# Optimization experiments

Measured on AMD Instinct MI355X. Metric: run time of the kernel, lower is better.

Reference implementation:

```python
import jax, jax.numpy as jnp
import numpy as np

# --- module hyperparams (match init_kwargs) ---
IN_F, OUT_F, K, GROUP, STRIDE, PAD = 64, 64, 3, 8, 1, 1
NUM_KERNELS = int(np.ceil(OUT_F / GROUP))          # 8 groups
IN_DPC = int(np.ceil(IN_F / NUM_KERNELS))          # in-ch per group = 8
WORKING = GROUP * NUM_KERNELS                      # 64 conv out channels
WORKING_IN = IN_DPC * NUM_KERNELS                  # 64 conv in channels
B, H, W = 16, 192, 192


def setup_inputs() -> dict:
    key = jax.random.key(0)
    k1, k2, k3, k4, k5, k6 = jax.random.split(key, 6)
    x = jax.random.normal(k1, (B, IN_F, H, W), jnp.float32)
    # grouped conv weight, torch layout (out, in/groups, kh, kw), no bias
    conv_w = jax.random.normal(k2, (WORKING, WORKING_IN // NUM_KERNELS, K, K), jnp.float32) * 0.05
    A = jax.random.uniform(k3, (1, WORKING, 1, 1), jnp.float32)
    D = jax.random.uniform(k4, (1, WORKING, 1, 1), jnp.float32)
    bias = jax.random.uniform(k5, (1, WORKING, 1, 1), jnp.float32)
    perm = jax.random.permutation(k6, WORKING).astype(jnp.int32)  # torch.randperm buffer
    return {"x": x, "conv_w": conv_w, "A": A, "D": D, "bias": bias, "perm": perm}


def reference(x, conv_w, A, D, bias, perm):
    # channel pad to working_in (no-op for these dims, kept for fidelity)
    z = jnp.pad(x, ((0, 0), (0, WORKING_IN - IN_F), (0, 0), (0, 0)))
    # grouped conv2d, no bias
    z = jax.lax.conv_general_dilated(
        z, conv_w,
        window_strides=(STRIDE, STRIDE),
        padding=((PAD, PAD), (PAD, PAD)),
        dimension_numbers=("NCHW", "OIHW", "NCHW"),
        feature_group_count=NUM_KERNELS,
    )
    z = z * A                      # elementwise scale
    z = jnp.fft.fft(z, axis=1)     # FFT along channel dim -> complex64
    z = z * D                      # diagonal (real) scale in frequency space
    z = jnp.fft.ifft(z, axis=1)    # back to 'channel' space (still complex)
    z = z + bias
    # channel permutation gather, slice to out_f, normalize
    z = jnp.take(z, perm, axis=1)[:, :OUT_F]
    return z / jnp.sqrt(jnp.float32(OUT_F))
```

## Files before the change

kernel.cpp:

```cpp
#include <hip/hip_runtime.h>
#include <math.h>

#define Bn 16
#define Cn 64
#define Hn 192
#define Wn 192
#define NPIX (Bn * Cn * Hn * Wn)
#define NBLKS 256
#define ROWS 12
#define SLOTB (194 * 128)

typedef short bf16x8 __attribute__((ext_vector_type(8)));
typedef float f32x4 __attribute__((ext_vector_type(4)));
typedef __attribute__((address_space(1))) const unsigned int as1_u32;
typedef __attribute__((address_space(3))) unsigned int as3_u32;

__device__ __align__(16) unsigned short g_Ms[9 * 64 * 64];
__device__ __align__(16) float g_b2[64];

static __device__ __forceinline__ unsigned short f2bf(float f) {
    union { float f; unsigned u; } x; x.f = f;
    unsigned r = x.u + 0x7fffu + ((x.u >> 16) & 1u);
    return (unsigned short)(r >> 16);
}

__global__ void acdc_precompute(const float* __restrict__ cw, const float* __restrict__ A,
                                const float* __restrict__ D, const float* __restrict__ bias,
                                const int* __restrict__ perm) {
    __shared__ float mre[64];
    int p = blockIdx.x;
    int t = threadIdx.x;
    if (t < 64) {
        float re = 0.f;
        for (int k = 0; k < 64; ++k) {
            int a = (k * t) & 63;
            re += D[k] * cosf((float)a * 0.0981747704246810387f);
        }
        mre[t] = re;
    }
    __syncthreads();
    int pp = perm[p];
    for (int k0 = t; k0 < 576; k0 += 256) {
        int sp = k0 >> 6, c = k0 & 63;
        int g = c >> 3, cil = c & 7;
        float val = 0.f;
        for (int o = 0; o < 8; ++o) {
            int oc = g * 8 + o;
            float gco = mre[(pp - oc + 64) & 63] * A[oc] * (0.125f / 64.0f);
            val += gco * cw[(oc * 8 + cil) * 9 + sp];
        }
        g_Ms[((sp * 64 + p) << 6) + (((g ^ (p & 7)) << 3) | cil)] = f2bf(val);
    }
    if (p == 0 && t < 64)
        g_b2[t] = bias[perm[t]] * 0.125f;
}

__global__ __launch_bounds__(1024)
void acdc_main(const float* __restrict__ x, float* __restrict__ out) {
    __shared__ __align__(16) unsigned short Mlds[9 * 64 * 64];
    __shared__ __align__(16) unsigned char xsb[3 * SLOTB];

    int tid = threadIdx.x;
    int lane = tid & 63, wv = tid >> 6;
    int Lb = (blockIdx.x & 7) * (NBLKS / 8) + (blockIdx.x >> 3);
    int bb = Lb >> 4;
    int h0 = (Lb & 15) * ROWS;

    #pragma unroll
    for (int k = 0; k < 5; ++k) {
        int chunk = wv + k * 16;
        if (chunk < 72) {
            const unsigned char* src = (const unsigned char*)g_Ms + chunk * 1024 + lane * 16;
            __builtin_amdgcn_global_load_lds((as1_u32*)(const void*)src,
                (as3_u32*)(void*)((unsigned char*)Mlds + chunk * 1024), 16, 0, 0);
        }
    }

    int pxw = lane & 15, q = lane >> 4, rlane = lane & 15;
    int m = wv >> 2;
    int ng = wv & 3;

    const float* xb = x + (size_t)bb * Cn * Hn * Wn;

    float4 va[2], vb[2];
    auto xload = [&](int gh) {
        bool ok = (unsigned)gh < (unsigned)Hn;
        int ghc = ok ? gh : 0;
        #pragma unroll
        for (int k = 0; k < 2; ++k) {
            int idx = tid + (k << 10);
            va[k] = (float4){0.f, 0.f, 0.f, 0.f};
            vb[k] = (float4){0.f, 0.f, 0.f, 0.f};
            if (idx < 1600) {
                int f = idx % 50;
                int cp = idx / 50;
                if (ok && f >= 1 && f <= 48) {
                    const float* r0 = xb + ((size_t)(2 * cp) * Hn + ghc) * Wn + (f * 4 - 4);
                    va[k] = *(const float4*)r0;
                    vb[k] = *(const float4*)(r0 + Hn * Wn);
                }
            }
        }
    };
    auto xwrite = [&](int slot) {
        #pragma unroll
        for (int k = 0; k < 2; ++k) {
            int idx = tid + (k << 10);
            if (idx >= 1600) break;
            int f = idx % 50;
            int cp = idx / 50;
            int chunk = cp >> 2, sub = (cp & 3) * 4;
            float v0[4] = {va[k].x, va[k].y, va[k].z, va[k].w};
            float v1[4] = {vb[k].x, vb[k].y, vb[k].z, vb[k].w};
            #pragma unroll
            for (int j = 0; j < 4; ++j) {
                int c2 = f * 4 - 3 + j;
                if ((unsigned)c2 >= 194u) continue;
                unsigned u;
                asm("v_cvt_pk_bf16_f32 %0, %1, %2" : "=v"(u) : "v"(v0[j]), "v"(v1[j]));
                int key = (c2 + (c2 >> 3) + 3 * slot) & 7;
                int byte = slot * SLOTB + c2 * 128 + ((chunk ^ key) << 4) + sub;
                *(unsigned*)(xsb + byte) = u;
            }
        }
    };

    xload(h0 - 1); xwrite(0);
    xload(h0);     xwrite(1);
    xload(h0 + 1); xwrite(2);
    __syncthreads();

    int sA = 0;
    for (int t = 0; t < ROWS; ++t) {
        int h = h0 + t;
        int sB = sA + 1; if (sB == 3) sB = 0;
        int sC = sB + 1; if (sC == 3) sC = 0;
        if (t < ROWS - 1) xload(h + 2);

        f32x4 acc[3];
        #pragma unroll
        for (int i = 0; i < 3; ++i) acc[i] = (f32x4){0.f, 0.f, 0.f, 0.f};

        #pragma unroll
        for (int sp = 0; sp < 9; ++sp) {
            const int dy = sp / 3, dx = sp % 3;
            int slotr = (dy == 0) ? sA : (dy == 1) ? sB : sC;
            int sb = slotr * SLOTB;
            int s3 = 3 * slotr;
            int c2b = ng * 16 + pxw + dx;
            #pragma unroll
            for (int kh = 0; kh < 2; ++kh) {
                int ksl = kh * 4 + q;
                bf16x8 am = *(const bf16x8*)((const unsigned char*)Mlds + sp * 8192 +
                             rlane * 128 + ((ksl ^ (rlane & 7)) << 4) + m * 2048);
                bf16x8 bfr[3];
                #pragma unroll
                for (int i = 0; i < 3; ++i) {
                    int c2 = c2b + i * 64;
                    int key = (c2 + (c2 >> 3) + s3) & 7;
                    bfr[i] = *(const bf16x8*)(xsb + sb + c2 * 128 + ((ksl ^ key) << 4));
                }
                __builtin_amdgcn_s_setprio(1);
                #pragma unroll
                for (int i = 0; i < 3; ++i)
                    acc[i] = __builtin_amdgcn_mfma_f32_16x16x32_bf16(am, bfr[i], acc[i], 0, 0, 0);
                __builtin_amdgcn_s_setprio(0);
            }
        }

        {
            int rbase = m * 16 + q * 4;
            float4 bq = *(const float4*)(g_b2 + rbase);
            float bvs[4] = {bq.x, bq.y, bq.z, bq.w};
            #pragma unroll
            for (int i = 0; i < 3; ++i) {
                int px = (ng + i * 4) * 16 + pxw;
                #pragma unroll
                for (int j = 0; j < 4; ++j)
                    out[(((size_t)(bb * Cn + rbase + j)) * Hn + h) * Wn + px] =
                        acc[i][j] + bvs[j];
            }
        }

        __syncthreads();
        if (t < ROWS - 1) xwrite(sA);
        __syncthreads();
        sA = sB;
    }
}

extern "C" void kernel_launch(void* const* d_in, const int* in_sizes, int n_in,
                              void* d_out, int out_size, void* d_ws, size_t ws_size,
                              hipStream_t stream) {
    const float* x    = (const float*)d_in[0];
    const float* cw   = (const float*)d_in[1];
    const float* A    = (const float*)d_in[2];
    const float* D    = (const float*)d_in[3];
    const float* bias = (const float*)d_in[4];
    const int*   perm = (const int*)d_in[5];

    acdc_precompute<<<dim3(64), dim3(256), 0, stream>>>(cw, A, D, bias, perm);
    acdc_main<<<dim3(NBLKS), dim3(1024), 0, stream>>>(x, (float*)d_out);
}
```

Baseline: 92.16 us.

## Split row bands into column halves and compute four rows per step

The grid doubles to 512 blocks, and each block now covers a 96-column half of a 12-row band. Each iteration computes four output rows at once: waves are assigned per row, and each wave handles two M tiles against three pixel tiles. The ring grows to six LDS slots and is refilled four rows at a time, so there are 3 iterations instead of 12. This cuts barrier and loop overhead and reuses each A fragment across more MFMAs. The cost is extra halo columns at the split, scalar edge loads and more registers.

Measured after the change: 166.9 us. 1.81x slower.

```diff
diff --git a/kernel.cpp b/kernel.cpp
--- a/kernel.cpp
+++ b/kernel.cpp
@@ -6,9 +6,9 @@
 #define Hn 192
 #define Wn 192
 #define NPIX (Bn * Cn * Hn * Wn)
-#define NBLKS 256
-#define ROWS 12
-#define SLOTB (194 * 128)
+#define NBLKS 512
+#define WCOLS 98
+#define SLOTB (WCOLS * 128)
 
 typedef short bf16x8 __attribute__((ext_vector_type(8)));
 typedef float f32x4 __attribute__((ext_vector_type(4)));
@@ -58,13 +58,16 @@
 __global__ __launch_bounds__(1024)
 void acdc_main(const float* __restrict__ x, float* __restrict__ out) {
     __shared__ __align__(16) unsigned short Mlds[9 * 64 * 64];
-    __shared__ __align__(16) unsigned char xsb[3 * SLOTB];
+    __shared__ __align__(16) unsigned char xsb[6 * SLOTB];
 
     int tid = threadIdx.x;
     int lane = tid & 63, wv = tid >> 6;
     int Lb = (blockIdx.x & 7) * (NBLKS / 8) + (blockIdx.x >> 3);
-    int bb = Lb >> 4;
-    int h0 = (Lb & 15) * ROWS;
+    int bb = Lb >> 5;
+    int band = (Lb >> 1) & 15;
+    int half = Lb & 1;
+    int h0 = band * 12;
+    int cbase = half * 96;
 
     #pragma unroll
     for (int k = 0; k < 5; ++k) {
@@ -77,115 +80,173 @@
     }
 
     int pxw = lane & 15, q = lane >> 4, rlane = lane & 15;
-    int m = wv >> 2;
-    int ng = wv & 3;
+    int r = wv & 3;
+    int mg = (wv >> 2) & 1;
+    int ngg = wv >> 3;
 
     const float* xb = x + (size_t)bb * Cn * Hn * Wn;
 
-    float4 va[2], vb[2];
-    auto xload = [&](int gh) {
-        bool ok = (unsigned)gh < (unsigned)Hn;
-        int ghc = ok ? gh : 0;
+    for (int k = 0; k < 5; ++k) {
+        int idx = tid + (k << 10);
+        if (idx >= 4992) break;
+        int f = idx % 26;
+        int rr = (idx / 26) % 6;
+        int cp = idx / 156;
+        int gi = h0 - 1 + rr;
+        int gc0 = cbase - 4 + 4 * f;
+        float av[4] = {0.f, 0.f, 0.f, 0.f}, bv[4] = {0.f, 0.f, 0.f, 0.f};
+        bool giok = (unsigned)gi < (unsigned)Hn;
+        const float* r0 = xb + ((size_t)(2 * cp) * Hn + (giok ? gi : 0)) * Wn;
+        const float* r1 = r0 + Hn * Wn;
+        if (giok) {
+            if (gc0 >= 0 && gc0 <= Wn - 4) {
+                float4 a = *(const float4*)(r0 + gc0);
+                float4 b = *(const float4*)(r1 + gc0);
+                av[0]=a.x; av[1]=a.y; av[2]=a.z; av[3]=a.w;
+                bv[0]=b.x; bv[1]=b.y; bv[2]=b.z; bv[3]=b.w;
+            } else {
+                #pragma unroll
+                for (int j = 0; j < 4; ++j) {
+                    int gc = gc0 + j;
+                    if ((unsigned)gc < (unsigned)Wn) { av[j] = r0[gc]; bv[j] = r1[gc]; }
+                }
+            }
+        }
+        int slot = rr;
+        int chunk = cp >> 2, sub = (cp & 3) * 4;
         #pragma unroll
-        for (int k = 0; k < 2; ++k) {
-            int idx = tid + (k << 10);
-            va[k] = (float4){0.f, 0.f, 0.f, 0.f};
-            vb[k] = (float4){0.f, 0.f, 0.f, 0.f};
-            if (idx < 1600) {
-                int f = idx % 50;
-                int cp = idx / 50;
-                if (ok && f >= 1 && f <= 48) {
-                    const float* r0 = xb + ((size_t)(2 * cp) * Hn + ghc) * Wn + (f * 4 - 4);
-                    va[k] = *(const float4*)r0;
-                    vb[k] = *(const float4*)(r0 + Hn * Wn);
-                }
-            }
-        }
-    };
-    auto xwrite = [&](int slot) {
+        for (int j = 0; j < 4; ++j) {
+            int c2 = 4 * f + j - 3;
+            if ((unsigned)c2 >= (unsigned)WCOLS) continue;
+            unsigned u;
+            asm("v_cvt_pk_bf16_f32 %0, %1, %2" : "=v"(u) : "v"(av[j]), "v"(bv[j]));
+            int key = (c2 + (c2 >> 3) + 3 * slot) & 7;
+            *(unsigned*)(xsb + slot * SLOTB + c2 * 128 + ((chunk ^ key) << 4) + sub) = u;
+        }
+    }
+    __syncthreads();
+
+    float4 va[4], vb[4];
+    for (int t = 0; t < 3; ++t) {
+        int hb = h0 + 4 * t;
+        int S = (t == 0) ? 0 : (t == 1) ? 4 : 2;
+
+        if (t < 2) {
+            #pragma unroll
+            for (int k = 0; k < 4; ++k) {
+                int idx = tid + (k << 10);
+                va[k] = (float4){0.f,0.f,0.f,0.f};
+                vb[k] = (float4){0.f,0.f,0.f,0.f};
+                if (idx >= 3328) continue;
+                int f = idx % 26;
+                int rr = (idx / 26) & 3;
+                int cp = idx / 104;
+                int gi = hb + 5 + rr;
+                int gc0 = cbase - 4 + 4 * f;
+                bool giok = (unsigned)gi < (unsigned)Hn;
+                const float* r0 = xb + ((size_t)(2 * cp) * Hn + (giok ? gi : 0)) * Wn;
+                const float* r1 = r0 + Hn * Wn;
+                if (giok) {
+                    if (gc0 >= 0 && gc0 <= Wn - 4) {
+                        va[k] = *(const float4*)(r0 + gc0);
+                        vb[k] = *(const float4*)(r1 + gc0);
+                    } else {
+                        float t0[4] = {0,0,0,0}, t1[4] = {0,0,0,0};
+                        #pragma unroll
+                        for (int j = 0; j < 4; ++j) {
+                            int gc = gc0 + j;
+                            if ((unsigned)gc < (unsigned)Wn) { t0[j] = r0[gc]; t1[j] = r1[gc]; }
+                        }
+                        va[k] = (float4){t0[0], t0[1], t0[2], t0[3]};
+                        vb[k] = (float4){t1[0], t1[1], t1[2], t1[3]};
+                    }
+                }
+            }
+        }
+
+        f32x4 acc[2][3];
         #pragma unroll
-        for (int k = 0; k < 2; ++k) {
-            int idx = tid + (k << 10);
-            if (idx >= 1600) break;
-            int f = idx % 50;
-            int cp = idx / 50;
-            int chunk = cp >> 2, sub = (cp & 3) * 4;
-            float v0[4] = {va[k].x, va[k].y, va[k].z, va[k].w};
-            float v1[4] = {vb[k].x, vb[k].y, vb[k].z, vb[k].w};
-            #pragma unroll
-            for (int j = 0; j < 4; ++j) {
-                int c2 = f * 4 - 3 + j;
-                if ((unsigned)c2 >= 194u) continue;
-                unsigned u;
-                asm("v_cvt_pk_bf16_f32 %0, %1, %2" : "=v"(u) : "v"(v0[j]), "v"(v1[j]));
-                int key = (c2 + (c2 >> 3) + 3 * slot) & 7;
-                int byte = slot * SLOTB + c2 * 128 + ((chunk ^ key) << 4) + sub;
-                *(unsigned*)(xsb + byte) = u;
-            }
-        }
-    };
-
-    xload(h0 - 1); xwrite(0);
-    xload(h0);     xwrite(1);
-    xload(h0 + 1); xwrite(2);
-    __syncthreads();
-
-    int sA = 0;
-    for (int t = 0; t < ROWS; ++t) {
-        int h = h0 + t;
-        int sB = sA + 1; if (sB == 3) sB = 0;
-        int sC = sB + 1; if (sC == 3) sC = 0;
-        if (t < ROWS - 1) xload(h + 2);
-
-        f32x4 acc[3];
-        #pragma unroll
-        for (int i = 0; i < 3; ++i) acc[i] = (f32x4){0.f, 0.f, 0.f, 0.f};
+        for (int mi = 0; mi < 2; ++mi)
+            #pragma unroll
+            for (int i = 0; i < 3; ++i)
+                acc[mi][i] = (f32x4){0.f, 0.f, 0.f, 0.f};
 
         #pragma unroll
         for (int sp = 0; sp < 9; ++sp) {
             const int dy = sp / 3, dx = sp % 3;
-            int slotr = (dy == 0) ? sA : (dy == 1) ? sB : sC;
-            int sb = slotr * SLOTB;
-            int s3 = 3 * slotr;
-            int c2b = ng * 16 + pxw + dx;
+            int v = S + r + dy; if (v >= 6) v -= 6;
+            int sb = v * SLOTB;
+            int k3 = 3 * v;
+            int c2base = ngg * 48 + pxw + dx;
             #pragma unroll
             for (int kh = 0; kh < 2; ++kh) {
                 int ksl = kh * 4 + q;
-                bf16x8 am = *(const bf16x8*)((const unsigned char*)Mlds + sp * 8192 +
-                             rlane * 128 + ((ksl ^ (rlane & 7)) << 4) + m * 2048);
+                const unsigned char* mrow = (const unsigned char*)Mlds + sp * 8192 +
+                                            rlane * 128 + ((ksl ^ (rlane & 7)) << 4);
+                bf16x8 am0 = *(const bf16x8*)(mrow + (2 * mg) * 2048);
+                bf16x8 am1 = *(const bf16x8*)(mrow + (2 * mg + 1) * 2048);
                 bf16x8 bfr[3];
                 #pragma unroll
                 for (int i = 0; i < 3; ++i) {
-                    int c2 = c2b + i * 64;
-                    int key = (c2 + (c2 >> 3) + s3) & 7;
+                    int c2 = c2base + i * 16;
+                    int key = (c2 + (c2 >> 3) + k3) & 7;
                     bfr[i] = *(const bf16x8*)(xsb + sb + c2 * 128 + ((ksl ^ key) << 4));
                 }
                 __builtin_amdgcn_s_setprio(1);
                 #pragma unroll
                 for (int i = 0; i < 3; ++i)
-                    acc[i] = __builtin_amdgcn_mfma_f32_16x16x32_bf16(am, bfr[i], acc[i], 0, 0, 0);
+                    acc[0][i] = __builtin_amdgcn_mfma_f32_16x16x32_bf16(am0, bfr[i], acc[0][i], 0, 0, 0);
+                #pragma unroll
+                for (int i = 0; i < 3; ++i)
+                    acc[1][i] = __builtin_amdgcn_mfma_f32_16x16x32_bf16(am1, bfr[i], acc[1][i], 0, 0, 0);
                 __builtin_amdgcn_s_setprio(0);
             }
         }
 
         {
-            int rbase = m * 16 + q * 4;
-            float4 bq = *(const float4*)(g_b2 + rbase);
-            float bvs[4] = {bq.x, bq.y, bq.z, bq.w};
-            #pragma unroll
-            for (int i = 0; i < 3; ++i) {
-                int px = (ng + i * 4) * 16 + pxw;
-                #pragma unroll
-                for (int j = 0; j < 4; ++j)
-                    out[(((size_t)(bb * Cn + rbase + j)) * Hn + h) * Wn + px] =
-                        acc[i][j] + bvs[j];
+            int h = hb + r;
+            #pragma unroll
+            for (int mi = 0; mi < 2; ++mi) {
+                int rbase = (2 * mg + mi) * 16 + q * 4;
+                float4 bq = *(const float4*)(g_b2 + rbase);
+                float bvs[4] = {bq.x, bq.y, bq.z, bq.w};
+                #pragma unroll
+                for (int i = 0; i < 3; ++i) {
+                    int px = cbase + ngg * 48 + i * 16 + pxw;
+                    #pragma unroll
+                    for (int jj = 0; jj < 4; ++jj)
+                        out[(((size_t)(bb * Cn + rbase + jj)) * Hn + h) * Wn + px] =
+                            acc[mi][i][jj] + bvs[jj];
+                }
             }
         }
 
         __syncthreads();
-        if (t < ROWS - 1) xwrite(sA);
+
+        if (t < 2) {
+            #pragma unroll
+            for (int k = 0; k < 4; ++k) {
+                int idx = tid + (k << 10);
+                if (idx >= 3328) continue;
+                int f = idx % 26;
+                int rr = (idx / 26) & 3;
+                int cp = idx / 104;
+                int vslot = S + rr; if (vslot >= 6) vslot -= 6;
+                int chunk = cp >> 2, sub = (cp & 3) * 4;
+                float v0[4] = {va[k].x, va[k].y, va[k].z, va[k].w};
+                float v1[4] = {vb[k].x, vb[k].y, vb[k].z, vb[k].w};
+                #pragma unroll
+                for (int j = 0; j < 4; ++j) {
+                    int c2 = 4 * f + j - 3;
+                    if ((unsigned)c2 >= (unsigned)WCOLS) continue;
+                    unsigned u;
+                    asm("v_cvt_pk_bf16_f32 %0, %1, %2" : "=v"(u) : "v"(v0[j]), "v"(v1[j]));
+                    int key = (c2 + (c2 >> 3) + 3 * vslot) & 7;
+                    *(unsigned*)(xsb + vslot * SLOTB + c2 * 128 + ((chunk ^ key) << 4) + sub) = u;
+                }
+            }
+        }
         __syncthreads();
-        sA = sB;
     }
 }
 
```
